# Kernel tuning notes

Hardware: AMD Instinct MI355X
Metric: run time of the kernel (lower is better)

## Reference

```python
import jax, jax.numpy as jnp
import numpy as np

IMG_W = 512.0
IMG_H = 512.0
LOC_VARIANCE = (0.1, 0.1, 0.2, 0.2)
IOU_THRESHOLD = 0.5
SCORE_THRESHOLD = 0.02
MAX_DETECTIONS = 100
NUM_ANCHORS = 200000
NUM_CLASSES = 91  # includes background class 0


def setup_inputs() -> dict:
    key = jax.random.key(0)
    k1, k2, k3 = jax.random.split(key, 3)
    predictions = jax.random.normal(k1, (1, NUM_ANCHORS, 4 + NUM_CLASSES), dtype=jnp.float32)
    # default boxes in (cx, cy, w, h), roughly inside a 512x512 image
    cxy = jax.random.uniform(k2, (NUM_ANCHORS, 2), dtype=jnp.float32) * IMG_W
    wh = jax.random.uniform(k3, (NUM_ANCHORS, 2), dtype=jnp.float32) * 96.0 + 8.0
    default_boxes = jnp.concatenate([cxy, wh], axis=-1)
    return {"predictions": predictions, "default_boxes": default_boxes}


def _greedy_nms(boxes, scores_work, max_det, iou_thr):
    # boxes: [N,4] corners; scores_work: [N] with invalid entries = -inf
    n = boxes.shape[0]
    areas = (boxes[:, 2] - boxes[:, 0]) * (boxes[:, 3] - boxes[:, 1])
    arange_n = jnp.arange(n)

    def body(i, state):
        sw, idxs, valid = state
        j = jnp.argmax(sw)
        ok = sw[j] > -jnp.inf
        box = boxes[j]
        lt = jnp.maximum(box[:2], boxes[:, :2])
        rb = jnp.minimum(box[2:], boxes[:, 2:])
        whd = jnp.clip(rb - lt, 0.0, None)
        inter = whd[:, 0] * whd[:, 1]
        iou = inter / (areas[j] + areas - inter + 1e-9)
        suppress = (iou > iou_thr) | (arange_n == j)
        sw = jnp.where(ok & suppress, -jnp.inf, sw)
        idxs = idxs.at[i].set(jnp.where(ok, j, 0))
        valid = valid.at[i].set(ok)
        return sw, idxs, valid

    idxs0 = jnp.zeros((max_det,), dtype=jnp.int32)
    valid0 = jnp.zeros((max_det,), dtype=bool)
    _, idxs, valid = jax.lax.fori_loop(0, max_det, body, (scores_work, idxs0, valid0))
    return idxs, valid


def reference(predictions, default_boxes):
    preds = predictions[0]  # [N, 4 + C]
    var = jnp.asarray(LOC_VARIANCE, dtype=preds.dtype)
    loc = preds[:, :4] * var
    cls = jax.nn.softmax(preds[:, 4:], axis=-1)

    # decode cxcywh
    cxy = loc[:, :2] * default_boxes[:, 2:] + default_boxes[:, :2]
    wh = jnp.exp(loc[:, 2:]) * default_boxes[:, 2:]
    corners = jnp.concatenate([cxy - 0.5 * wh, cxy + 0.5 * wh], axis=-1)
    lims = jnp.asarray([IMG_W, IMG_H, IMG_W, IMG_H], dtype=corners.dtype)
    boxes = jnp.clip(corners, 0.0, lims)  # [N,4] x1,y1,x2,y2

    cls_ids = jnp.argmax(cls, axis=-1)
    cls_scores = jnp.max(cls, axis=-1)

    # background filter + score threshold, expressed as masking (fixed shapes)
    fg = cls_ids != 0
    scores_work = jnp.where(fg & (cls_scores >= SCORE_THRESHOLD), cls_scores, -jnp.inf)

    nms_idx, valid = _greedy_nms(boxes, scores_work, MAX_DETECTIONS, IOU_THRESHOLD)

    dec_boxes = jnp.where(valid[:, None], boxes[nms_idx], 0.0)
    dec_ids = jnp.where(valid, cls_ids[nms_idx] - 1, -1)
    dec_scores = jnp.where(valid, cls_scores[nms_idx], 0.0)
    return dec_boxes, dec_ids, dec_scores
```

## Files before the change

kernel.cpp:

```cpp
#include <hip/hip_runtime.h>
#include <stdint.h>

#define N_ANCHORS   200000
#define NUM_CLASSES 91
#define PRED_STRIDE 95
#define TILE_BYTES  24320
#define MAX_DET     100
#define CAP         4096
#define M_TARGET    3600
#define NBUCKETS    65536
#define NREP        8
#define N_TILES     3125

__device__ __forceinline__ void gload_lds16(const void* g, void* l) {
  __builtin_amdgcn_global_load_lds(
      (const __attribute__((address_space(1))) uint32_t*)g,
      (__attribute__((address_space(3))) uint32_t*)l, 16, 0, 0);
}

__global__ __launch_bounds__(256) void zero_kernel(unsigned int* __restrict__ hist,
                                                   int* __restrict__ ctr) {
  int i = blockIdx.x * 256 + threadIdx.x;
  if (i < NREP * NBUCKETS) hist[i] = 0u;
  if (i == 0) ctr[0] = 0;
}

__global__ __launch_bounds__(128) void decode_kernel(
    const float* __restrict__ pred, const float* __restrict__ dbx,
    float4* __restrict__ boxes, unsigned long long* __restrict__ keys,
    unsigned int* __restrict__ hist)
{
  __shared__ float tile[2][64 * PRED_STRIDE];
  const int wv   = threadIdx.x >> 6;
  const int lane = threadIdx.x & 63;
  const int w    = blockIdx.x * 2 + wv;
  if (w >= N_TILES) return;
  float* T = tile[wv];
  const char* src = (const char*)pred + (size_t)w * TILE_BYTES;

#pragma unroll
  for (int q = 0; q < 23; ++q)
    gload_lds16(src + q * 1024 + lane * 16, &T[q * 256]);
  gload_lds16(src + 23296 + lane * 16, &T[5824]);
  asm volatile("s_waitcnt vmcnt(0)" ::: "memory");
  __builtin_amdgcn_sched_barrier(0);

  const float* R = T + lane * PRED_STRIDE;

  float m = R[4]; int am = 0;
#pragma unroll
  for (int j = 1; j < NUM_CLASSES; ++j) {
    float v = R[4 + j];
    if (v > m) { m = v; am = j; }
  }
  float s = 0.f;
#pragma unroll
  for (int j = 0; j < NUM_CLASSES; ++j) s += expf(R[4 + j] - m);
  float score = 1.0f / s;

  const int gi = w * 64 + lane;
  float4 d = ((const float4*)dbx)[gi];
  float lx = R[0] * 0.1f, ly = R[1] * 0.1f, lw = R[2] * 0.2f, lh = R[3] * 0.2f;
  float cx = lx * d.z + d.x;
  float cy = ly * d.w + d.y;
  float bw = expf(lw) * d.z;
  float bh = expf(lh) * d.w;
  float x1 = fminf(fmaxf(cx - 0.5f * bw, 0.f), 512.f);
  float y1 = fminf(fmaxf(cy - 0.5f * bh, 0.f), 512.f);
  float x2 = fminf(fmaxf(cx + 0.5f * bw, 0.f), 512.f);
  float y2 = fminf(fmaxf(cy + 0.5f * bh, 0.f), 512.f);
  boxes[gi] = make_float4(x1, y1, x2, y2);

  bool valid = (am != 0) && (score >= 0.02f);
  unsigned int sb = __float_as_uint(score);
  unsigned int payload = ~(((unsigned int)gi << 7) | (unsigned int)am);
  unsigned long long key = valid ? (((unsigned long long)sb << 32) | payload) : 0ull;
  keys[gi] = key;
  if (valid) atomicAdd(&hist[(w & (NREP - 1)) * NBUCKETS + (sb >> 16)], 1u);
}

__global__ __launch_bounds__(256) void chunksum_kernel(
    const unsigned int* __restrict__ hist, unsigned int* __restrict__ chunksum)
{
  int tid = blockIdx.x * 256 + threadIdx.x;
  int W = tid >> 6, lane = tid & 63;
  unsigned int s = 0;
#pragma unroll
  for (int r = 0; r < NREP; ++r) s += hist[r * NBUCKETS + W * 64 + lane];
  for (int off = 32; off; off >>= 1) s += __shfl_down(s, off);
  if (lane == 0) chunksum[W] = s;
}

__global__ __launch_bounds__(1024) void thresh_kernel(
    const unsigned int* __restrict__ hist, const unsigned int* __restrict__ chunksum,
    unsigned int* __restrict__ thr)
{
  __shared__ unsigned int csum[1024];
  __shared__ unsigned int cbuf[64];
  __shared__ int cstar;
  __shared__ unsigned int cafter;
  int t = threadIdx.x;
  csum[t] = chunksum[t];
  if (t == 0) cstar = -1;
  __syncthreads();
  for (int off = 1; off < 1024; off <<= 1) {
    unsigned int v = (t + off < 1024) ? csum[t + off] : 0u;
    __syncthreads();
    csum[t] += v;
    __syncthreads();
  }
  unsigned int mine  = csum[t];
  unsigned int after = (t == 1023) ? 0u : csum[t + 1];
  if (mine >= M_TARGET && (t == 1023 || after < M_TARGET)) {
    cstar = t; cafter = after;
  }
  if (t == 0 && csum[0] < M_TARGET) thr[0] = 0u;
  __syncthreads();
  if (t < 64 && cstar >= 0) {
    int b = cstar * 64 + t;
    unsigned int cnt = 0;
#pragma unroll
    for (int r = 0; r < NREP; ++r) cnt += hist[r * NBUCKETS + b];
    cbuf[t] = cnt;
  }
  __syncthreads();
  if (t == 0 && cstar >= 0) {
    unsigned int running = cafter;
    unsigned int thrv = 0u;
    for (int i = 63; i >= 0; --i) {
      running += cbuf[i];
      if (running >= M_TARGET) {
        unsigned int b = (unsigned int)(cstar * 64 + i);
        thrv = (running > CAP) ? ((b + 1) << 16) : (b << 16);
        break;
      }
    }
    thr[0] = thrv;
  }
}

__global__ __launch_bounds__(256) void compact_kernel(
    const unsigned long long* __restrict__ keys, const unsigned int* __restrict__ thr,
    unsigned long long* __restrict__ cand, int* __restrict__ ctr)
{
  int i = blockIdx.x * 256 + threadIdx.x;
  if (i >= N_ANCHORS) return;
  unsigned long long k = keys[i];
  if (k != 0ull) {
    unsigned int sb = (unsigned int)(k >> 32);
    if (sb >= thr[0]) {
      int pos = atomicAdd(ctr, 1);
      if (pos < CAP) cand[pos] = k;
    }
  }
}

__global__ __launch_bounds__(1024) void nms_kernel(
    const unsigned long long* __restrict__ cand, const int* __restrict__ ctr,
    const float4* __restrict__ boxes, float* __restrict__ out)
{
  __shared__ unsigned long long sk[CAP];
  __shared__ float4 abox[MAX_DET];
  __shared__ float aarea[MAX_DET];
  __shared__ unsigned long long akey[MAX_DET];
  __shared__ int acount;

  int K = ctr[0]; if (K > CAP) K = CAP;
  for (int t = threadIdx.x; t < CAP; t += 1024)
    sk[t] = (t < K) ? cand[t] : 0ull;
  __syncthreads();

  for (int k = 2; k <= CAP; k <<= 1) {
    for (int j = k >> 1; j > 0; j >>= 1) {
      for (int t = threadIdx.x; t < CAP; t += 1024) {
        int l = t ^ j;
        if (l > t) {
          unsigned long long a = sk[t], b = sk[l];
          bool up = ((t & k) == 0);
          bool sw = up ? (a < b) : (a > b);
          if (sw) { sk[t] = b; sk[l] = a; }
        }
      }
      __syncthreads();
    }
  }
  __syncthreads();

  if (threadIdx.x < 64) {
    int lane = threadIdx.x;
    int ac = 0;
    for (int gbase = 0; gbase < CAP && ac < MAX_DET; gbase += 64) {
      if (gbase >= K) break;
      __asm__ __volatile__("" ::: "memory");
      unsigned long long key = sk[gbase + lane];
      bool alive = (key != 0ull);
      float4 b = make_float4(0.f, 0.f, 0.f, 0.f);
      float area = 0.f;
      if (alive) {
        unsigned int pay = ~(unsigned int)key;
        int idx = (int)(pay >> 7);
        b = boxes[idx];
        area = (b.z - b.x) * (b.w - b.y);
      }
      for (int a2 = 0; a2 < ac; ++a2) {
        if (alive) {
          float4 ab = abox[a2];
          float lx = fmaxf(ab.x, b.x), ly = fmaxf(ab.y, b.y);
          float rx = fminf(ab.z, b.z), ry = fminf(ab.w, b.w);
          float iw = fmaxf(rx - lx, 0.f), ih = fmaxf(ry - ly, 0.f);
          float inter = iw * ih;
          float iou = inter / (aarea[a2] + area - inter + 1e-9f);
          if (iou > 0.5f) alive = false;
        }
      }
      while (ac < MAX_DET) {
        unsigned long long mv = __ballot(alive);
        if (mv == 0ull) break;
        int first = __ffsll(mv) - 1;
        float wx1 = __shfl(b.x, first), wy1 = __shfl(b.y, first);
        float wx2 = __shfl(b.z, first), wy2 = __shfl(b.w, first);
        float wa  = __shfl(area, first);
        if (lane == first) {
          abox[ac] = b; aarea[ac] = area; akey[ac] = key;
          alive = false;
        }
        __asm__ __volatile__("" ::: "memory");
        if (alive) {
          float lx = fmaxf(wx1, b.x), ly = fmaxf(wy1, b.y);
          float rx = fminf(wx2, b.z), ry = fminf(wy2, b.w);
          float iw = fmaxf(rx - lx, 0.f), ih = fmaxf(ry - ly, 0.f);
          float inter = iw * ih;
          float iou = inter / (wa + area - inter + 1e-9f);
          if (iou > 0.5f) alive = false;
        }
        ++ac;
      }
    }
    if (lane == 0) acount = ac;
  }
  __syncthreads();

  int t = threadIdx.x;
  if (t < MAX_DET) {
    float bx1 = 0.f, by1 = 0.f, bx2 = 0.f, by2 = 0.f, idf = -1.f, sc = 0.f;
    if (t < acount) {
      unsigned long long key = akey[t];
      float4 b = abox[t];
      bx1 = b.x; by1 = b.y; bx2 = b.z; by2 = b.w;
      unsigned int pay = ~(unsigned int)key;
      int clsid = (int)(pay & 0x7Fu);
      idf = (float)(clsid - 1);
      sc = __uint_as_float((unsigned int)(key >> 32));
    }
    out[t * 4 + 0] = bx1; out[t * 4 + 1] = by1;
    out[t * 4 + 2] = bx2; out[t * 4 + 3] = by2;
    out[400 + t] = idf;
    out[500 + t] = sc;
  }
}

extern "C" void kernel_launch(void* const* d_in, const int* in_sizes, int n_in,
                              void* d_out, int out_size, void* d_ws, size_t ws_size,
                              hipStream_t stream) {
  (void)in_sizes; (void)n_in; (void)out_size; (void)ws_size;
  const float* pred = (const float*)d_in[0];
  const float* dbx  = (const float*)d_in[1];
  float* out = (float*)d_out;

  char* ws = (char*)d_ws;
  float4*             boxes = (float4*)(ws);
  unsigned long long* keys  = (unsigned long long*)(ws + 3200000);
  unsigned int*       hist  = (unsigned int*)(ws + 4800000);
  unsigned int*       csums = (unsigned int*)(ws + 6897152);
  int*                ctr   = (int*)(ws + 6901248);
  unsigned int*       thr   = (unsigned int*)(ws + 6901264);
  unsigned long long* cand  = (unsigned long long*)(ws + 6901280);

  hipLaunchKernelGGL(zero_kernel, dim3((NREP * NBUCKETS) / 256), dim3(256), 0, stream,
                     hist, ctr);
  hipLaunchKernelGGL(decode_kernel, dim3((N_TILES + 1) / 2), dim3(128), 0, stream,
                     pred, dbx, boxes, keys, hist);
  hipLaunchKernelGGL(chunksum_kernel, dim3(NBUCKETS / 256), dim3(256), 0, stream,
                     hist, csums);
  hipLaunchKernelGGL(thresh_kernel, dim3(1), dim3(1024), 0, stream,
                     hist, csums, thr);
  hipLaunchKernelGGL(compact_kernel, dim3((N_ANCHORS + 255) / 256), dim3(256), 0, stream,
                     keys, thr, cand, ctr);
  hipLaunchKernelGGL(nms_kernel, dim3(1), dim3(1024), 0, stream,
                     cand, ctr, boxes, out);
}
```

Before: 252.9 us.

## Register-resident bitonic sort with wave shuffles and in-thread exchanges

Replaces the shared-memory bitonic sort of the candidate keys with one where each thread holds four keys in registers. Stages with stride below 256 use intra-wave xor shuffles or in-thread compare-exchange and need no barrier; only large strides go through LDS with barriers. This is meant to cut the many __syncthreads and LDS round trips in the NMS kernel's sort, at the cost of more complex indexing logic that must match the original descending order.

```diff
diff --git a/kernel.cpp b/kernel.cpp
--- a/kernel.cpp
+++ b/kernel.cpp
@@ -16,6 +16,22 @@
   __builtin_amdgcn_global_load_lds(
       (const __attribute__((address_space(1))) uint32_t*)g,
       (__attribute__((address_space(3))) uint32_t*)l, 16, 0, 0);
+}
+
+__device__ __forceinline__ unsigned long long umax64(unsigned long long a,
+                                                     unsigned long long b) {
+  return a > b ? a : b;
+}
+__device__ __forceinline__ unsigned long long umin64(unsigned long long a,
+                                                     unsigned long long b) {
+  return a < b ? a : b;
+}
+__device__ __forceinline__ void cex(unsigned long long& a, unsigned long long& b,
+                                    bool up) {
+  unsigned long long mx = a > b ? a : b;
+  unsigned long long mn = a > b ? b : a;
+  a = up ? mx : mn;
+  b = up ? mn : mx;
 }
 
 __global__ __launch_bounds__(256) void zero_kernel(unsigned int* __restrict__ hist,
@@ -165,25 +181,52 @@
   __shared__ unsigned long long akey[MAX_DET];
   __shared__ int acount;
 
+  const int t = threadIdx.x;
   int K = ctr[0]; if (K > CAP) K = CAP;
-  for (int t = threadIdx.x; t < CAP; t += 1024)
-    sk[t] = (t < K) ? cand[t] : 0ull;
-  __syncthreads();
+
+  unsigned long long r0, r1, r2, r3;
+  {
+    const int b = 4 * t;
+    r0 = (b + 0 < K) ? cand[b + 0] : 0ull;
+    r1 = (b + 1 < K) ? cand[b + 1] : 0ull;
+    r2 = (b + 2 < K) ? cand[b + 2] : 0ull;
+    r3 = (b + 3 < K) ? cand[b + 3] : 0ull;
+  }
 
   for (int k = 2; k <= CAP; k <<= 1) {
     for (int j = k >> 1; j > 0; j >>= 1) {
-      for (int t = threadIdx.x; t < CAP; t += 1024) {
-        int l = t ^ j;
-        if (l > t) {
-          unsigned long long a = sk[t], b = sk[l];
-          bool up = ((t & k) == 0);
-          bool sw = up ? (a < b) : (a > b);
-          if (sw) { sk[t] = b; sk[l] = a; }
-        }
-      }
-      __syncthreads();
-    }
-  }
+      const bool up = (((4 * t) & k) == 0);
+      if (j >= 256) {
+        sk[4 * t + 0] = r0; sk[4 * t + 1] = r1;
+        sk[4 * t + 2] = r2; sk[4 * t + 3] = r3;
+        __syncthreads();
+        const int pt = 4 * (t ^ (j >> 2));
+        unsigned long long p0 = sk[pt + 0], p1 = sk[pt + 1];
+        unsigned long long p2 = sk[pt + 2], p3 = sk[pt + 3];
+        const bool takemax = (up == ((t & (j >> 2)) == 0));
+        r0 = takemax ? umax64(r0, p0) : umin64(r0, p0);
+        r1 = takemax ? umax64(r1, p1) : umin64(r1, p1);
+        r2 = takemax ? umax64(r2, p2) : umin64(r2, p2);
+        r3 = takemax ? umax64(r3, p3) : umin64(r3, p3);
+        __syncthreads();
+      } else if (j >= 4) {
+        const int lx = j >> 2;
+        const bool takemax = (up == ((t & lx) == 0));
+        unsigned long long p;
+        p = __shfl_xor(r0, lx); r0 = takemax ? umax64(r0, p) : umin64(r0, p);
+        p = __shfl_xor(r1, lx); r1 = takemax ? umax64(r1, p) : umin64(r1, p);
+        p = __shfl_xor(r2, lx); r2 = takemax ? umax64(r2, p) : umin64(r2, p);
+        p = __shfl_xor(r3, lx); r3 = takemax ? umax64(r3, p) : umin64(r3, p);
+      } else if (j == 2) {
+        cex(r0, r2, up); cex(r1, r3, up);
+      } else {
+        if (k == 2) { cex(r0, r1, true); cex(r2, r3, false); }
+        else        { cex(r0, r1, up);   cex(r2, r3, up);   }
+      }
+    }
+  }
+  sk[4 * t + 0] = r0; sk[4 * t + 1] = r1;
+  sk[4 * t + 2] = r2; sk[4 * t + 3] = r3;
   __syncthreads();
 
   if (threadIdx.x < 64) {
@@ -240,7 +283,6 @@
   }
   __syncthreads();
 
-  int t = threadIdx.x;
   if (t < MAX_DET) {
     float bx1 = 0.f, by1 = 0.f, bx2 = 0.f, by2 = 0.f, idf = -1.f, sc = 0.f;
     if (t < acount) {
```

Measured after the change: 220.3 us. -12.9%, faster.
